# Optimization experiments

Hardware: AMD Instinct MI355X
Metric: run time of the kernel (lower is better)

## Reference

```python
import jax, jax.numpy as jnp
import numpy as np

N_NODES = 100000
N_EDGES = 1600000
DIM = 128
NUM_HEADS = 8
HEAD_DIM = DIM // NUM_HEADS


def setup_inputs() -> dict:
    key = jax.random.key(0)
    k_x, k_src, k_dst, k_wqkv, k_bqkv, k_wout, k_bout = jax.random.split(key, 7)
    x = jax.random.normal(k_x, (N_NODES, DIM), dtype=jnp.float32)
    src = jax.random.randint(k_src, (N_EDGES,), 0, N_NODES, dtype=jnp.int32)
    dst = jax.random.randint(k_dst, (N_EDGES,), 0, N_NODES, dtype=jnp.int32)
    s = 1.0 / np.sqrt(DIM)
    Wqkv = jax.random.uniform(k_wqkv, (DIM, 3 * DIM), jnp.float32, -s, s)
    bqkv = jax.random.uniform(k_bqkv, (3 * DIM,), jnp.float32, -s, s)
    Wout = jax.random.uniform(k_wout, (DIM, DIM), jnp.float32, -s, s)
    bout = jax.random.uniform(k_bout, (DIM,), jnp.float32, -s, s)
    return {"x": x, "Wqkv": Wqkv, "bqkv": bqkv, "Wout": Wout, "bout": bout,
            "src": src, "dst": dst}


def reference(x, Wqkv, bqkv, Wout, bout, src, dst):
    n = x.shape[0]
    scale = 1.0 / np.sqrt(HEAD_DIM)
    # QKV projection -> [N, H, 3*hd], split exactly like torch .split on last dim
    qkv = (x @ Wqkv + bqkv).reshape(n, NUM_HEADS, 3 * HEAD_DIM)
    q = qkv[..., :HEAD_DIM]                       # queries  [N, H, hd]
    k = qkv[..., HEAD_DIM:2 * HEAD_DIM]           # keys     [N, H, hd]
    v = qkv[..., 2 * HEAD_DIM:]                   # values   [N, H, hd]
    # u_dot_v: per edge (u=src, v=dst): dot(keys[u], queries[v]) per head
    scores = jnp.einsum('ehd,ehd->eh', k[src], q[dst]) * scale  # [E, H]
    # edge_softmax over incoming edges of each dst node
    m = jax.ops.segment_max(scores, dst, num_segments=n)        # [N, H]
    p = jnp.exp(scores - m[dst])                                # [E, H]
    denom = jax.ops.segment_sum(p, dst, num_segments=n)         # [N, H]
    probs = p / denom[dst]                                      # [E, H]
    # u_mul_e_sum: scatter-sum of values[src] * probs into dst
    msgs = v[src] * probs[:, :, None]                            # [E, H, hd]
    agg = jax.ops.segment_sum(msgs, dst, num_segments=n)         # [N, H, hd]
    out = agg.reshape(n, DIM) @ Wout + bout
    return out
```

## Files before the change

kernel.cpp:

```cpp
#include <hip/hip_runtime.h>
#include <cstdint>
#include <cstddef>

#define N_DIM 128
#define QKV_DIM 384
#define NUM_HEADS 8
#define HEAD_DIM 16
#define SCAN_B 256
#define SCAN_V 4
#define SCAN_TILE (SCAN_B * SCAN_V)

typedef unsigned int uint;
typedef unsigned short ushort;
typedef __attribute__((ext_vector_type(8))) short short8;
typedef __attribute__((ext_vector_type(4))) float f32x4;

__device__ __forceinline__ ushort f2bf(float f) {
    uint u = __float_as_uint(f);
    uint r = u + 0x7fffu + ((u >> 16) & 1u);
    return (ushort)(r >> 16);
}
__device__ __forceinline__ float bf_lo(uint u) { return __uint_as_float(u << 16); }
__device__ __forceinline__ float bf_hi(uint u) { return __uint_as_float(u & 0xffff0000u); }

__global__ void pack_w_kernel(const float* __restrict__ Wq, const float* __restrict__ Wo,
                              ushort* __restrict__ WpQ, ushort* __restrict__ WpO) {
    int idx = blockIdx.x * blockDim.x + threadIdx.x;
    const float* W;
    ushort* Wp;
    int N;
    if (idx < 128 * QKV_DIM) {
        W = Wq; Wp = WpQ; N = QKV_DIM;
    } else {
        idx -= 128 * QKV_DIM;
        if (idx >= 128 * N_DIM) return;
        W = Wo; Wp = WpO; N = N_DIM;
    }
    int j = idx & 7;
    int l = (idx >> 3) & 63;
    int fs = idx >> 9;
    int T = fs >> 2, s = fs & 3;
    int k = s * 32 + (l >> 4) * 8 + j;
    int c = T * 16 + (l & 15);
    Wp[idx] = f2bf(W[k * N + c]);
}

__global__ __launch_bounds__(256) void qkv_gemm(const float* __restrict__ x,
                                                const ushort* __restrict__ Wp,
                                                const float* __restrict__ bqkv,
                                                float* __restrict__ qtab,
                                                ushort* __restrict__ kvb,
                                                const int* __restrict__ dst,
                                                int* __restrict__ counts,
                                                int n, int nE) {
    {
        int stride = gridDim.x * blockDim.x;
        for (int e = blockIdx.x * blockDim.x + threadIdx.x; e < nE; e += stride)
            atomicAdd(&counts[dst[e]], 1);
    }
    __shared__ float  lq[4][16][64];
    __shared__ ushort lkv[4][16][128];
    int w = threadIdx.x >> 6, lane = threadIdx.x & 63;
    int node0 = blockIdx.x * 64 + w * 16;
    int m = lane & 15, quad = lane >> 4;
    int arow = node0 + m; if (arow >= n) arow = n - 1;
    const float* xr = x + (size_t)arow * N_DIM;
    short8 A[4];
    #pragma unroll
    for (int s = 0; s < 4; ++s) {
        float4 f0 = *(const float4*)(xr + s * 32 + quad * 8);
        float4 f1 = *(const float4*)(xr + s * 32 + quad * 8 + 4);
        uint u0 = (uint)f2bf(f0.x) | ((uint)f2bf(f0.y) << 16);
        uint u1 = (uint)f2bf(f0.z) | ((uint)f2bf(f0.w) << 16);
        uint u2 = (uint)f2bf(f1.x) | ((uint)f2bf(f1.y) << 16);
        uint u3 = (uint)f2bf(f1.z) | ((uint)f2bf(f1.w) << 16);
        uint4 u = make_uint4(u0, u1, u2, u3);
        A[s] = *(short8*)&u;
    }
    for (int half = 0; half < 2; ++half) {
        for (int T12 = 0; T12 < 12; ++T12) {
            int T = half * 12 + T12;
            f32x4 acc = {0.f, 0.f, 0.f, 0.f};
            const ushort* bp = Wp + ((size_t)(T * 4) * 64 + lane) * 8;
            #pragma unroll
            for (int s = 0; s < 4; ++s) {
                uint4 u = *(const uint4*)(bp + s * 512);
                short8 B = *(short8*)&u;
                acc = __builtin_amdgcn_mfma_f32_16x16x32_bf16(A[s], B, acc, 0, 0, 0);
            }
            int c = T * 16 + m;
            int hq = T / 3, wvv = T % 3;
            int hl = hq - half * 4;
            float bb = bqkv[c];
            #pragma unroll
            for (int r = 0; r < 4; ++r) {
                int nd16 = quad * 4 + r;
                float v = acc[r] + bb;
                if (wvv == 0) lq[w][nd16][hl * 16 + m] = v;
                else          lkv[w][nd16][hl * 32 + (wvv - 1) * 16 + m] = f2bf(v);
            }
        }
        #pragma unroll
        for (int rr = 0; rr < 4; ++rr) {
            int of = rr * 256 + lane * 4;
            int ndq = of >> 6, colq = of & 63;
            float4 qv = *(const float4*)&lq[w][ndq][colq];
            int gq = node0 + ndq;
            if (gq < n)
                *(float4*)(qtab + (size_t)gq * N_DIM + half * 64 + colq) = qv;
            int ou = rr * 512 + lane * 8;
            int ndk = ou >> 7, elk = ou & 127;
            uint4 kvv = *(const uint4*)&lkv[w][ndk][elk];
            int gk = node0 + ndk;
            if (gk < n)
                *(uint4*)(kvb + (size_t)gk * 256 + half * 128 + elk) = kvv;
        }
    }
}

__global__ __launch_bounds__(256) void out_gemm(const uint* __restrict__ aggb,
                                                const ushort* __restrict__ Wp,
                                                const float* __restrict__ bout,
                                                float* __restrict__ out, int n) {
    int w = threadIdx.x >> 6, lane = threadIdx.x & 63;
    int node0 = blockIdx.x * 64 + w * 16;
    int m = lane & 15, quad = lane >> 4;
    int arow = node0 + m; if (arow >= n) arow = n - 1;
    const uint* ar = aggb + (size_t)arow * 64;
    short8 A[4];
    #pragma unroll
    for (int s = 0; s < 4; ++s) {
        uint4 u = *(const uint4*)(ar + s * 16 + quad * 4);
        A[s] = *(short8*)&u;
    }
    for (int T = 0; T < 8; ++T) {
        f32x4 acc = {0.f, 0.f, 0.f, 0.f};
        const ushort* bp = Wp + ((size_t)(T * 4) * 64 + lane) * 8;
        #pragma unroll
        for (int s = 0; s < 4; ++s) {
            uint4 u = *(const uint4*)(bp + s * 512);
            short8 B = *(short8*)&u;
            acc = __builtin_amdgcn_mfma_f32_16x16x32_bf16(A[s], B, acc, 0, 0, 0);
        }
        int c = T * 16 + m;
        float bb = bout[c];
        #pragma unroll
        for (int r = 0; r < 4; ++r) {
            int nd = node0 + quad * 4 + r;
            if (nd < n) out[(size_t)nd * N_DIM + c] = acc[r] + bb;
        }
    }
}

__global__ void scan1_kernel(const int* __restrict__ counts, int* __restrict__ offs,
                             int* __restrict__ partials, int n) {
    __shared__ int ts[SCAN_B];
    int t = threadIdx.x;
    int base = blockIdx.x * SCAN_TILE + t * SCAN_V;
    int v[SCAN_V];
    int s = 0;
    #pragma unroll
    for (int i = 0; i < SCAN_V; ++i) { v[i] = (base + i < n) ? counts[base + i] : 0; s += v[i]; }
    ts[t] = s;
    __syncthreads();
    for (int off = 1; off < SCAN_B; off <<= 1) {
        int x = (t >= off) ? ts[t - off] : 0;
        __syncthreads();
        ts[t] += x;
        __syncthreads();
    }
    int run = (t > 0) ? ts[t - 1] : 0;
    if (t == SCAN_B - 1) partials[blockIdx.x] = ts[SCAN_B - 1];
    #pragma unroll
    for (int i = 0; i < SCAN_V; ++i) { if (base + i < n) offs[base + i] = run; run += v[i]; }
}

__global__ void scan2_kernel(int* __restrict__ partials, int P) {
    __shared__ int ps[1024];
    int t = threadIdx.x;
    ps[t] = (t < P) ? partials[t] : 0;
    __syncthreads();
    for (int off = 1; off < 1024; off <<= 1) {
        int x = (t >= off) ? ps[t - off] : 0;
        __syncthreads();
        ps[t] += x;
        __syncthreads();
    }
    if (t < P) partials[t] = (t > 0) ? ps[t - 1] : 0;
}

__global__ void scan3_kernel(int* __restrict__ offs, const int* __restrict__ partials,
                             int* __restrict__ cursor, int n, int nE) {
    int i = blockIdx.x * blockDim.x + threadIdx.x;
    if (i < n) {
        int o = offs[i] + partials[i / SCAN_TILE];
        offs[i] = o;
        cursor[i] = o;
    }
    if (i == 0) offs[n] = nE;
}

__global__ __launch_bounds__(256) void scatter_src_shard(const int* __restrict__ src,
                                                         const int* __restrict__ dst,
                                                         int* __restrict__ cursor,
                                                         int* __restrict__ esrc,
                                                         int nE, int shardSize) {
    int shard = blockIdx.x & 7;
    int sub   = blockIdx.x >> 3;
    int nsub  = gridDim.x >> 3;
    int lo = shard * shardSize;
    int hi = lo + shardSize;
    int stride = nsub * blockDim.x;
    for (int e = sub * blockDim.x + threadIdx.x; e < nE; e += stride) {
        int d = dst[e];
        if (d >= lo && d < hi) {
            int pos = atomicAdd(&cursor[d], 1);
            esrc[pos] = src[e];
        }
    }
}

__global__ void attn_kernel(const float* __restrict__ qtab, const uint* __restrict__ kvu,
                            const int* __restrict__ esrc, const int* __restrict__ offs,
                            ushort* __restrict__ aggb, int n) {
    int node = blockIdx.x;
    int t = threadIdx.x;
    __shared__ float qs[16][8];
    __shared__ uint  so[16];
    __shared__ float pp[16][8];
    __shared__ float lw[2][8];
    int h  = t >> 4, dd = t & 15;
    int h2 = t & 7,  el = t >> 3;
    {
        float qv = qtab[(size_t)node * N_DIM + t];
        qs[dd][h] = qv;
    }
    int start = offs[node];
    int deg = offs[node + 1] - start;
    float lsum = 0.f, acc = 0.f;
    uint voffb = (uint)h * 64u + 32u + (uint)(dd >> 1) * 4u;
    bool hi = (dd & 1);
    __syncthreads();

    for (int c0 = 0; c0 < deg; c0 += 16) {
        int rem = deg - c0;
        int cn = rem < 16 ? rem : 16;
        if (t < 16) so[t] = (t < cn) ? ((uint)esrc[start + c0 + t] << 9) : 0u;
        __syncthreads();
        float pv = 0.f;
        if (el < cn) {
            const uint* kr = (const uint*)((const char*)kvu + so[el] + (uint)h2 * 64u);
            uint4 A = *((const uint4*)kr);
            uint4 B = *((const uint4*)(kr + 4));
            float dot = 0.f;
            dot = fmaf(bf_lo(A.x), qs[0][h2],  dot); dot = fmaf(bf_hi(A.x), qs[1][h2],  dot);
            dot = fmaf(bf_lo(A.y), qs[2][h2],  dot); dot = fmaf(bf_hi(A.y), qs[3][h2],  dot);
            dot = fmaf(bf_lo(A.z), qs[4][h2],  dot); dot = fmaf(bf_hi(A.z), qs[5][h2],  dot);
            dot = fmaf(bf_lo(A.w), qs[6][h2],  dot); dot = fmaf(bf_hi(A.w), qs[7][h2],  dot);
            dot = fmaf(bf_lo(B.x), qs[8][h2],  dot); dot = fmaf(bf_hi(B.x), qs[9][h2],  dot);
            dot = fmaf(bf_lo(B.y), qs[10][h2], dot); dot = fmaf(bf_hi(B.y), qs[11][h2], dot);
            dot = fmaf(bf_lo(B.z), qs[12][h2], dot); dot = fmaf(bf_hi(B.z), qs[13][h2], dot);
            dot = fmaf(bf_lo(B.w), qs[14][h2], dot); dot = fmaf(bf_hi(B.w), qs[15][h2], dot);
            pv = __expf(dot * 0.25f);
        }
        pp[el][h2] = pv;
        lsum += pv;
        __syncthreads();
        float vacc = 0.f;
        if (cn == 16) {
            uint vv[16];
            #pragma unroll
            for (int i = 0; i < 16; ++i)
                vv[i] = *(const uint*)((const char*)kvu + (so[i] + voffb));
            #pragma unroll
            for (int i = 0; i < 16; ++i) {
                float p = pp[i][h];
                float v = hi ? bf_hi(vv[i]) : bf_lo(vv[i]);
                vacc = fmaf(p, v, vacc);
            }
        } else {
            for (int i = 0; i < cn; ++i) {
                uint u = *(const uint*)((const char*)kvu + (so[i] + voffb));
                float p = pp[i][h];
                float v = hi ? bf_hi(u) : bf_lo(u);
                vacc = fmaf(p, v, vacc);
            }
        }
        acc += vacc;
        __syncthreads();
    }
    lsum += __shfl_xor(lsum, 8, 64);
    lsum += __shfl_xor(lsum, 16, 64);
    lsum += __shfl_xor(lsum, 32, 64);
    if ((t & 63) < 8) lw[t >> 6][t & 7] = lsum;
    __syncthreads();
    float L = lw[0][h] + lw[1][h];
    aggb[(size_t)node * N_DIM + t] = f2bf((L > 0.f) ? acc / L : 0.f);
}

extern "C" void kernel_launch(void* const* d_in, const int* in_sizes, int n_in,
                              void* d_out, int out_size, void* d_ws, size_t ws_size,
                              hipStream_t stream) {
    const float* x    = (const float*)d_in[0];
    const float* Wqkv = (const float*)d_in[1];
    const float* bqkv = (const float*)d_in[2];
    const float* Wout = (const float*)d_in[3];
    const float* bout = (const float*)d_in[4];
    const int*   src  = (const int*)d_in[5];
    const int*   dst  = (const int*)d_in[6];
    float* out = (float*)d_out;

    const int n  = in_sizes[0] / N_DIM;
    const int nE = in_sizes[5];

    uint* ws = (uint*)d_ws;
    float*  qtab   = (float*)ws;
    uint*   kvu    = ws + (size_t)n * 128;
    uint*   aggb   = kvu + (size_t)n * 128;
    ushort* WpQ    = (ushort*)(aggb + (size_t)n * 64);
    ushort* WpO    = WpQ + 128 * QKV_DIM;
    int*    counts = (int*)(WpO + 128 * N_DIM);
    int*    offs   = counts + n;
    int*    cursor = offs + n + 1;
    int*    partials = cursor + n;
    int*    esrc   = partials + 1024;

    hipMemsetAsync(counts, 0, (size_t)n * sizeof(int), stream);

    pack_w_kernel<<<(128 * (QKV_DIM + N_DIM) + 255) / 256, 256, 0, stream>>>(Wqkv, Wout, WpQ, WpO);

    qkv_gemm<<<(n + 63) / 64, 256, 0, stream>>>(x, WpQ, bqkv, qtab, (ushort*)kvu,
                                                dst, counts, n, nE);

    int P = (n + SCAN_TILE - 1) / SCAN_TILE;
    scan1_kernel<<<P, SCAN_B, 0, stream>>>(counts, offs, partials, n);
    scan2_kernel<<<1, 1024, 0, stream>>>(partials, P);
    scan3_kernel<<<(n + 255) / 256, 256, 0, stream>>>(offs, partials, cursor, n, nE);

    int shardSize = (n + 7) / 8;
    scatter_src_shard<<<8 * 128, 256, 0, stream>>>(src, dst, cursor, esrc, nE, shardSize);

    attn_kernel<<<n, 128, 0, stream>>>(qtab, kvu, esrc, offs, (ushort*)aggb, n);

    out_gemm<<<(n + 63) / 64, 256, 0, stream>>>(aggb, WpO, bout, out, n);
}
```

Before: 432.1 us.

## Cut attention barriers via shuffle-broadcast indices and double-buffered probabilities

```diff
diff --git a/kernel.cpp b/kernel.cpp
--- a/kernel.cpp
+++ b/kernel.cpp
@@ -225,10 +225,9 @@
                             ushort* __restrict__ aggb, int n) {
     int node = blockIdx.x;
     int t = threadIdx.x;
+    int l = t & 63;
     __shared__ float qs[16][8];
-    __shared__ uint  so[16];
-    __shared__ float pp[16][8];
-    __shared__ float lw[2][8];
+    __shared__ float pp[2][16][8];
     int h  = t >> 4, dd = t & 15;
     int h2 = t & 7,  el = t >> 3;
     {
@@ -237,19 +236,21 @@
     }
     int start = offs[node];
     int deg = offs[node + 1] - start;
-    float lsum = 0.f, acc = 0.f;
+    float lden = 0.f, acc = 0.f;
     uint voffb = (uint)h * 64u + 32u + (uint)(dd >> 1) * 4u;
     bool hi = (dd & 1);
     __syncthreads();
 
-    for (int c0 = 0; c0 < deg; c0 += 16) {
+    int par = 0;
+    for (int c0 = 0; c0 < deg; c0 += 16, par ^= 1) {
         int rem = deg - c0;
         int cn = rem < 16 ? rem : 16;
-        if (t < 16) so[t] = (t < cn) ? ((uint)esrc[start + c0 + t] << 9) : 0u;
-        __syncthreads();
+        uint sov = 0u;
+        if (l < 16 && l < cn) sov = (uint)esrc[start + c0 + l] << 9;
+        uint soA = __shfl(sov, el);
         float pv = 0.f;
         if (el < cn) {
-            const uint* kr = (const uint*)((const char*)kvu + so[el] + (uint)h2 * 64u);
+            const uint* kr = (const uint*)((const char*)kvu + soA + (uint)h2 * 64u);
             uint4 A = *((const uint4*)kr);
             uint4 B = *((const uint4*)(kr + 4));
             float dot = 0.f;
@@ -263,39 +264,36 @@
             dot = fmaf(bf_lo(B.w), qs[14][h2], dot); dot = fmaf(bf_hi(B.w), qs[15][h2], dot);
             pv = __expf(dot * 0.25f);
         }
-        pp[el][h2] = pv;
-        lsum += pv;
-        __syncthreads();
-        float vacc = 0.f;
+        pp[par][el][h2] = pv;
+        __syncthreads();
+        float vacc = 0.f, psum = 0.f;
         if (cn == 16) {
             uint vv[16];
             #pragma unroll
-            for (int i = 0; i < 16; ++i)
-                vv[i] = *(const uint*)((const char*)kvu + (so[i] + voffb));
+            for (int i = 0; i < 16; ++i) {
+                uint so_i = __shfl(sov, i);
+                vv[i] = *(const uint*)((const char*)kvu + (so_i + voffb));
+            }
             #pragma unroll
             for (int i = 0; i < 16; ++i) {
-                float p = pp[i][h];
+                float p = pp[par][i][h];
                 float v = hi ? bf_hi(vv[i]) : bf_lo(vv[i]);
                 vacc = fmaf(p, v, vacc);
+                psum += p;
             }
         } else {
             for (int i = 0; i < cn; ++i) {
-                uint u = *(const uint*)((const char*)kvu + (so[i] + voffb));
-                float p = pp[i][h];
-                float v = hi ? bf_hi(u) : bf_lo(u);
-                vacc = fmaf(p, v, vacc);
+                uint so_i = __shfl(sov, i);
+                uint u = *(const uint*)((const char*)kvu + (so_i + voffb));
+                float p = pp[par][i][h];
+                vacc = fmaf(p, hi ? bf_hi(u) : bf_lo(u), vacc);
+                psum += p;
             }
         }
         acc += vacc;
-        __syncthreads();
-    }
-    lsum += __shfl_xor(lsum, 8, 64);
-    lsum += __shfl_xor(lsum, 16, 64);
-    lsum += __shfl_xor(lsum, 32, 64);
-    if ((t & 63) < 8) lw[t >> 6][t & 7] = lsum;
-    __syncthreads();
-    float L = lw[0][h] + lw[1][h];
-    aggb[(size_t)node * N_DIM + t] = f2bf((L > 0.f) ? acc / L : 0.f);
+        lden += psum;
+    }
+    aggb[(size_t)node * N_DIM + t] = f2bf((lden > 0.f) ? acc / lden : 0.f);
 }
 
 extern "C" void kernel_launch(void* const* d_in, const int* in_sizes, int n_in,
```

Measured after the change: 443.0 us. 2.5% more time.
